# Kernel tuning notes

Hardware: AMD Instinct MI355X
Metric: run time of the kernel (lower is better)

The kernel has to match this reference:

```python
import jax, jax.numpy as jnp
import numpy as np

B, T, D, H = 4, 1024, 1024, 16
DK = D // H
SCALE = float(np.sqrt(DK))


def setup_inputs() -> dict:
    key = jax.random.key(0)
    ks = jax.random.split(key, 12)
    std = 1.0 / np.sqrt(D)
    inp = {
        "x": jax.random.normal(ks[0], (B, T, D), dtype=jnp.float32),
        "s2_distances": jax.random.uniform(ks[1], (B, T, T), dtype=jnp.float32),
        # causal mask: 1 where attention allowed (j <= i)
        "mask": jnp.broadcast_to(jnp.tril(jnp.ones((T, T), dtype=jnp.int32)), (B, T, T)),
        "Wq": jax.random.uniform(ks[2], (D, D), jnp.float32, -std, std),
        "bq": jax.random.uniform(ks[3], (D,), jnp.float32, -std, std),
        "Wk": jax.random.uniform(ks[4], (D, D), jnp.float32, -std, std),
        "bk": jax.random.uniform(ks[5], (D,), jnp.float32, -std, std),
        "Wv": jax.random.uniform(ks[6], (D, D), jnp.float32, -std, std),
        "bv": jax.random.uniform(ks[7], (D,), jnp.float32, -std, std),
        "Wo": jax.random.uniform(ks[8], (D, D), jnp.float32, -std, std),
        "bo": jax.random.uniform(ks[9], (D,), jnp.float32, -std, std),
        "spatial_weight": jnp.float32(0.5),
    }
    return inp


def reference(x, s2_distances, mask, Wq, bq, Wk, bk, Wv, bv, Wo, bo, spatial_weight):
    b, t, _ = x.shape
    # projections: torch nn.Linear is x @ W.T + b
    def proj(W, bias):
        y = jnp.einsum("btd,ed->bte", x, W) + bias
        return y.reshape(b, t, H, DK).transpose(0, 2, 1, 3)  # [B,H,T,dk]

    Q, K, V = proj(Wq, bq), proj(Wk, bk), proj(Wv, bv)
    # scores: QK^T/sqrt(dk) - |alpha| * dist  (dist broadcast over heads)
    scores = jnp.einsum("bhqd,bhkd->bhqk", Q, K) / SCALE
    scores = scores - jnp.abs(spatial_weight) * s2_distances[:, None, :, :]
    scores = jnp.where(mask[:, None, :, :] == 0, -jnp.inf, scores)
    probs = jax.nn.softmax(scores, axis=-1)
    out = jnp.einsum("bhqk,bhkd->bhqd", probs, V)
    out = out.transpose(0, 2, 1, 3).reshape(b, t, D)
    return jnp.einsum("btd,ed->bte", out, Wo) + bo
```

## Files before the change

### kernel.cpp

```cpp
#include <hip/hip_runtime.h>
#include <stdint.h>

#define Tt 1024
#define Dd 1024
#define Hh 16

typedef unsigned short u16;
typedef __attribute__((ext_vector_type(8))) short short8;
typedef __attribute__((ext_vector_type(4))) float f32x4;
typedef __attribute__((ext_vector_type(4))) unsigned short u16x4;

typedef const __attribute__((address_space(1))) uint32_t* gptr_t;
typedef __attribute__((address_space(3))) uint32_t* lptr_t;

#define QSCALE 0.18033688011112042f
#define LOG2E 1.4426950408889634f

static __device__ __forceinline__ u16 f2bf(float f) {
  union { float f; unsigned u; } x;
  x.f = f;
  unsigned u = x.u;
  return (u16)((u + 0x7fffu + ((u >> 16) & 1u)) >> 16);
}

static __device__ __forceinline__ u16 f2bf_fast(float f) {
  union { float f; unsigned u; } x;
  x.f = f;
  return (u16)((x.u + 0x8000u) >> 16);
}

static __device__ __forceinline__ float bf2f(u16 u) {
  union { unsigned u; float f; } x;
  x.u = ((unsigned)u) << 16;
  return x.f;
}

static __device__ __forceinline__ float fexp2(float x) {
#if __has_builtin(__builtin_amdgcn_exp2f)
  return __builtin_amdgcn_exp2f(x);
#else
  return exp2f(x);
#endif
}

__global__ __launch_bounds__(256) void cvt_kernel(
    const float* __restrict__ x, const float* __restrict__ wq,
    const float* __restrict__ wk, const float* __restrict__ wv,
    const float* __restrict__ wo, u16* __restrict__ xb, u16* __restrict__ wb) {
  size_t i = ((size_t)blockIdx.x * 256 + threadIdx.x) * 4;
  const size_t XN = (size_t)4 * 1024 * 1024;
  const float* src;
  u16* dst;
  size_t off;
  if (i < XN) {
    src = x; dst = xb; off = i;
  } else {
    size_t j = i - XN;
    int wi = (int)(j >> 20);
    src = (wi == 0) ? wq : (wi == 1) ? wk : (wi == 2) ? wv : wo;
    dst = wb + ((size_t)wi << 20);
    off = j & ((1u << 20) - 1);
  }
  float4 v = *(const float4*)(src + off);
  u16x4 o;
  o.x = f2bf(v.x); o.y = f2bf(v.y); o.z = f2bf(v.z); o.w = f2bf(v.w);
  *(u16x4*)(dst + off) = o;
}

__global__ __launch_bounds__(512, 2) void qkv_fused_kernel(
    const u16* __restrict__ xb, const u16* __restrict__ wb,
    const float* __restrict__ bq, const float* __restrict__ bk,
    const float* __restrict__ bv, u16* __restrict__ Q, u16* __restrict__ Kk,
    u16* __restrict__ Vt, const float* __restrict__ dist,
    const float* __restrict__ alphap, u16* __restrict__ biasb) {
  __shared__ u16 lds[65536];
  const int bid = blockIdx.x;
  if (bid >= 192) {
    const int cid = bid - 192;
    const float scl = -fabsf(alphap[0]) * LOG2E;
    const size_t id = (size_t)cid * 512 + threadIdx.x;
#pragma unroll 4
    for (int i = 0; i < 32; i++) {
      const size_t off = id * 4 + (size_t)i * 131072;
      float4 v = *(const float4*)(dist + off);
      u16x4 o;
      o.x = f2bf(v.x * scl); o.y = f2bf(v.y * scl);
      o.z = f2bf(v.z * scl); o.w = f2bf(v.w * scl);
      *(u16x4*)(biasb + off) = o;
    }
    return;
  }
  const int mt = bid & 15, ny = bid >> 4;
  const int z = ny >> 2;
  const int m0 = mt * 256, nc = (ny & 3) * 256;
  const u16* W = wb + ((size_t)z << 20);

  const int t = threadIdx.x, w = t >> 6, l = t & 63;
  const int quad = l >> 4, l15 = l & 15;
  const int wr = w >> 2, wn = w & 3;
  char* ldc = (char*)lds;

  const int srow = w * 16 + ((l >> 3) & 7);
  const int schunk = ((l & 7) ^ ((l >> 3) & 7)) * 8;
  const u16* gA = xb + (size_t)(m0 + srow) * Dd + schunk;
  const u16* gB = W + (size_t)(nc + srow) * Dd + schunk;

  auto stage = [&](int kt, int h) {
    const size_t ro = (size_t)(h * 128) * Dd + (size_t)kt * 64;
    char* base = ldc + ((((kt & 1) << 1) | h) * 32768) + w * 2048;
#pragma unroll
    for (int i = 0; i < 2; i++) {
      __builtin_amdgcn_global_load_lds((gptr_t)(gA + ro + (size_t)i * 8 * Dd),
                                       (lptr_t)(base + i * 1024), 16, 0, 0);
      __builtin_amdgcn_global_load_lds((gptr_t)(gB + ro + (size_t)i * 8 * Dd),
                                       (lptr_t)(base + 16384 + i * 1024), 16, 0, 0);
    }
  };

  f32x4 acc[8][4];
#pragma unroll
  for (int i = 0; i < 8; i++)
#pragma unroll
    for (int j = 0; j < 4; j++) acc[i][j] = (f32x4){0.f, 0.f, 0.f, 0.f};

  stage(0, 0); stage(0, 1);
  stage(1, 0); stage(1, 1);
  asm volatile("s_waitcnt vmcnt(8)" ::: "memory");
  __builtin_amdgcn_s_barrier();

  const int swl = l15 & 7;

#pragma unroll 1
  for (int kt = 0; kt < 16; kt++) {
    const char* slA = ldc + ((((kt & 1) << 1) | wr) * 32768);
    const char* slB = ldc + ((((kt & 1) << 1) | (wn >> 1)) * 32768) + 16384;
    const int rB = (wn & 1) * 64;
    {
      short8 af[8], bfv[4];
      const int cs = ((0 * 4 + quad) ^ swl) * 16;
#pragma unroll
      for (int mi = 0; mi < 8; mi++)
        af[mi] = *(const short8*)(slA + (mi * 16 + l15) * 128 + cs);
#pragma unroll
      for (int ni = 0; ni < 4; ni++)
        bfv[ni] = *(const short8*)(slB + (rB + ni * 16 + l15) * 128 + cs);
      __builtin_amdgcn_s_barrier();
      asm volatile("s_waitcnt lgkmcnt(0)" ::: "memory");
      __builtin_amdgcn_sched_barrier(0);
      __builtin_amdgcn_s_setprio(1);
#pragma unroll
      for (int mi = 0; mi < 8; mi++)
#pragma unroll
        for (int ni = 0; ni < 4; ni++)
          acc[mi][ni] = __builtin_amdgcn_mfma_f32_16x16x32_bf16(
              af[mi], bfv[ni], acc[mi][ni], 0, 0, 0);
      __builtin_amdgcn_s_setprio(0);
    }
    {
      short8 af[8], bfv[4];
      const int cs = ((1 * 4 + quad) ^ swl) * 16;
#pragma unroll
      for (int mi = 0; mi < 8; mi++)
        af[mi] = *(const short8*)(slA + (mi * 16 + l15) * 128 + cs);
#pragma unroll
      for (int ni = 0; ni < 4; ni++)
        bfv[ni] = *(const short8*)(slB + (rB + ni * 16 + l15) * 128 + cs);
      __builtin_amdgcn_s_barrier();
      if (kt + 2 < 16) { stage(kt + 2, 0); stage(kt + 2, 1); }
      asm volatile("s_waitcnt lgkmcnt(0)" ::: "memory");
      __builtin_amdgcn_sched_barrier(0);
      __builtin_amdgcn_s_setprio(1);
#pragma unroll
      for (int mi = 0; mi < 8; mi++)
#pragma unroll
        for (int ni = 0; ni < 4; ni++)
          acc[mi][ni] = __builtin_amdgcn_mfma_f32_16x16x32_bf16(
              af[mi], bfv[ni], acc[mi][ni], 0, 0, 0);
      __builtin_amdgcn_s_setprio(0);
      if (kt < 14) {
        asm volatile("s_waitcnt vmcnt(8)" ::: "memory");
      } else if (kt == 14) {
        asm volatile("s_waitcnt vmcnt(0)" ::: "memory");
      }
      if (kt < 15) __builtin_amdgcn_s_barrier();
    }
  }

  const float* bias = (z == 0) ? bq : (z == 1) ? bk : bv;
  const float scl = (z == 0) ? QSCALE : 1.0f;
  if (z < 2) {
#pragma unroll
    for (int mi = 0; mi < 8; mi++)
#pragma unroll
      for (int ni = 0; ni < 4; ni++) {
        const int n = wn * 64 + ni * 16 + l15;
        const float bn = bias[nc + n];
        const int nsw = n ^ (quad << 4);
#pragma unroll
        for (int r = 0; r < 4; r++) {
          const int m = wr * 128 + mi * 16 + quad * 4 + r;
          lds[m * 256 + nsw] = f2bf((acc[mi][ni][r] + bn) * scl);
        }
      }
  } else {
#pragma unroll
    for (int mi = 0; mi < 8; mi++)
#pragma unroll
      for (int ni = 0; ni < 4; ni++) {
        const int n = wn * 64 + ni * 16 + l15;
        const float bn = bias[nc + n];
        u16x4 o;
        o.x = f2bf(acc[mi][ni][0] + bn);
        o.y = f2bf(acc[mi][ni][1] + bn);
        o.z = f2bf(acc[mi][ni][2] + bn);
        o.w = f2bf(acc[mi][ni][3] + bn);
        const int mp = (wr * 128 + mi * 16 + quad * 4) ^ ((n & 7) * 8);
        *(u16x4*)&lds[n * 256 + mp] = o;
      }
  }
  __syncthreads();
  const int row = t >> 5;
  const int c8 = (t & 31) * 8;
  if (z < 2) {
    u16* out = (z == 0) ? Q : Kk;
#pragma unroll
    for (int it = 0; it < 16; it++) {
      const int rr = it * 16 + row;
      const int pos = c8 ^ ((((rr >> 2) & 3)) << 4);
      *(short8*)(out + (size_t)(m0 + rr) * Dd + nc + c8) =
          *(const short8*)&lds[rr * 256 + pos];
    }
  } else {
    const int b2 = m0 >> 10, t0 = m0 & (Tt - 1);
#pragma unroll
    for (int it = 0; it < 16; it++) {
      const int rr = it * 16 + row;
      const int pos = c8 ^ ((rr & 7) * 8);
      *(short8*)(Vt + ((size_t)b2 * Dd + nc + rr) * Tt + t0 + c8) =
          *(const short8*)&lds[rr * 256 + pos];
    }
  }
}

__global__ __launch_bounds__(512) void gemm_out_kernel(
    const u16* __restrict__ Ao, const u16* __restrict__ Wo,
    const float* __restrict__ bo, float* __restrict__ out) {
  __shared__ u16 lds[2 * 12288];
  const int m0 = blockIdx.x * 128, n0 = blockIdx.y * 64;
  const int t = threadIdx.x, w = t >> 6, l = t & 63, quad = l >> 4, l15 = l & 15;
  const int srow = t >> 3;
  const int scol = ((l & 7) ^ ((l >> 3) & 7)) * 8;
  const u16* ga = Ao + (size_t)(m0 + srow) * Dd + scol;
  const u16* gb = Wo + (size_t)(n0 + srow) * Dd + scol;
  char* ldc = (char*)lds;
  const int xr = l15 & 7;
  f32x4 acc[4];
#pragma unroll
  for (int j = 0; j < 4; j++) acc[j] = (f32x4){0.f, 0.f, 0.f, 0.f};

  auto stage = [&](int k0, int buf) {
    char* base = ldc + buf * 24576 + w * 1024;
#pragma unroll
    for (int i = 0; i < 2; i++)
      __builtin_amdgcn_global_load_lds((gptr_t)(ga + k0 + (size_t)i * 64 * Dd),
                                       (lptr_t)(base + i * 8192), 16, 0, 0);
    __builtin_amdgcn_global_load_lds((gptr_t)(gb + k0),
                                     (lptr_t)(base + 16384), 16, 0, 0);
  };

  stage(0, 0);
#pragma unroll 1
  for (int it = 0; it < Dd / 64; it++) {
    const int buf = it & 1;
    __builtin_amdgcn_s_waitcnt(0);
    __syncthreads();
    if (it + 1 < Dd / 64) stage((it + 1) * 64, buf ^ 1);
    const u16* lA = lds + buf * 12288;
    const u16* lB = lA + 8192;
#pragma unroll
    for (int kk = 0; kk < 2; kk++) {
      const int cs = ((kk * 4 + quad) ^ xr) * 8;
      const short8 af = *(const short8*)(lA + (w * 16 + l15) * 64 + cs);
#pragma unroll
      for (int ni = 0; ni < 4; ni++) {
        const short8 bfr = *(const short8*)(lB + (ni * 16 + l15) * 64 + cs);
        acc[ni] = __builtin_amdgcn_mfma_f32_16x16x32_bf16(af, bfr, acc[ni], 0, 0, 0);
      }
    }
  }
#pragma unroll
  for (int ni = 0; ni < 4; ni++) {
    const int n = n0 + ni * 16 + l15;
    const float bn = bo[n];
#pragma unroll
    for (int r = 0; r < 4; r++) {
      const int m = m0 + w * 16 + quad * 4 + r;
      out[(size_t)m * Dd + n] = acc[ni][r] + bn;
    }
  }
}

__global__ __launch_bounds__(256) void attn_kernel(
    const u16* __restrict__ Q, const u16* __restrict__ Kk,
    const u16* __restrict__ Vt, const u16* __restrict__ biasb,
    u16* __restrict__ Oo) {
  __shared__ u16 lK[2][64 * 64];
  __shared__ u16 lV[2][64 * 64];
  __shared__ u16 lPp[4][16 * 64];
  const int t = threadIdx.x, w = t >> 6, l = t & 63, quad = l >> 4, l15 = l & 15;
  const int g = blockIdx.x >> 8;
  const int j = (blockIdx.x >> 6) & 3;
  const int bh = blockIdx.x & 63;
  const int qb = (g == 0) ? 15 - j : (g == 1) ? 8 + j : (g == 2) ? 7 - j : j;
  const int h = bh & (Hh - 1), b = bh >> 4;
  const int q0 = qb * 64;

  const int srow = w * 8 + (l >> 3);
  const int schunk = ((l & 7) ^ ((l >> 3) & 7)) * 8;
  const u16* gK = Kk + ((size_t)b * Tt + srow) * Dd + h * 64 + schunk;
  const u16* gV = Vt + ((size_t)b * Dd + h * 64 + srow) * Tt + schunk;
  char* lKc0 = (char*)&lK[0][0];
  char* lVc0 = (char*)&lV[0][0];
  const int wbase = w * 1024;

  auto stage = [&](int k0, int buf) {
#pragma unroll
    for (int i = 0; i < 2; i++) {
      __builtin_amdgcn_global_load_lds(
          (gptr_t)(gK + (size_t)(k0 + i * 32) * Dd),
          (lptr_t)(lKc0 + buf * 8192 + wbase + i * 4096), 16, 0, 0);
      __builtin_amdgcn_global_load_lds(
          (gptr_t)(gV + (size_t)(i * 32) * Tt + k0),
          (lptr_t)(lVc0 + buf * 8192 + wbase + i * 4096), 16, 0, 0);
    }
  };

  const int qrow = q0 + w * 16 + l15;
  const u16* Qp = Q + ((size_t)b * Tt + qrow) * Dd + h * 64 + quad * 8;
  const short8 qf0 = *(const short8*)Qp;
  const short8 qf1 = *(const short8*)(Qp + 32);
  const u16* bp = biasb + ((size_t)b * Tt + qrow) * Tt + quad * 4;

  const int xr = l15 & 7;
  u16* lpr = &lPp[w][l15 * 64];
  const int niter = qb + 1;

  f32x4 oacc[4];
#pragma unroll
  for (int dt = 0; dt < 4; dt++) oacc[dt] = (f32x4){0.f, 0.f, 0.f, 0.f};
  f32x4 lsum4 = (f32x4){0.f, 0.f, 0.f, 0.f};
  u16x4 bbA[4], bbB[4];

  stage(0, 0);
#pragma unroll
  for (int nt = 0; nt < 4; nt++) bbA[nt] = *(const u16x4*)(bp + nt * 16);

#pragma unroll 1
  for (int kt = 0; kt < niter; kt++) {
    const int buf = kt & 1;
    __builtin_amdgcn_s_waitcnt(0);
    __syncthreads();
    if (kt + 1 < niter) {
      stage((kt + 1) * 64, buf ^ 1);
#pragma unroll
      for (int nt = 0; nt < 4; nt++)
        bbB[nt] = *(const u16x4*)(bp + (kt + 1) * 64 + nt * 16);
    }
    f32x4 sacc[4];
#pragma unroll
    for (int nt = 0; nt < 4; nt++) {
#pragma unroll
      for (int r = 0; r < 4; r++) sacc[nt][r] = bf2f(bbA[nt][r]);
    }
#pragma unroll
    for (int ks = 0; ks < 2; ks++) {
      const short8 qf = ks ? qf1 : qf0;
      const int cs = ((ks * 4 + quad) ^ xr) * 8;
#pragma unroll
      for (int nt = 0; nt < 4; nt++) {
        const short8 kf = *(const short8*)&lK[buf][(nt * 16 + l15) * 64 + cs];
        sacc[nt] = __builtin_amdgcn_mfma_f32_16x16x32_bf16(kf, qf, sacc[nt], 0, 0, 0);
      }
    }
    if (kt == qb) {
      const int kbase = kt * 64 + quad * 4;
#pragma unroll
      for (int nt = 0; nt < 4; nt++) {
        u16x4 pk;
#pragma unroll
        for (int r = 0; r < 4; r++) {
          const float p = (kbase + nt * 16 + r <= qrow) ? fexp2(sacc[nt][r]) : 0.f;
          lsum4[nt] += p;
          pk[r] = f2bf_fast(p);
        }
        *(u16x4*)&lpr[((nt * 4 + quad) ^ (xr << 1)) * 4] = pk;
      }
    } else {
#pragma unroll
      for (int nt = 0; nt < 4; nt++) {
        u16x4 pk;
#pragma unroll
        for (int r = 0; r < 4; r++) {
          const float p = fexp2(sacc[nt][r]);
          lsum4[nt] += p;
          pk[r] = f2bf_fast(p);
        }
        *(u16x4*)&lpr[((nt * 4 + quad) ^ (xr << 1)) * 4] = pk;
      }
    }
#pragma unroll
    for (int ks = 0; ks < 2; ks++) {
      const int cs = ((ks * 4 + quad) ^ xr) * 8;
      const short8 pa = *(const short8*)&lpr[cs];
#pragma unroll
      for (int dt = 0; dt < 4; dt++) {
        const short8 vf = *(const short8*)&lV[buf][(dt * 16 + l15) * 64 + cs];
        oacc[dt] = __builtin_amdgcn_mfma_f32_16x16x32_bf16(pa, vf, oacc[dt], 0, 0, 0);
      }
    }
#pragma unroll
    for (int nt = 0; nt < 4; nt++) bbA[nt] = bbB[nt];
  }

  float lsum = (lsum4[0] + lsum4[1]) + (lsum4[2] + lsum4[3]);
  lsum += __shfl_xor(lsum, 16);
  lsum += __shfl_xor(lsum, 32);
  const float inv = 1.0f / lsum;
  float invq[4];
#pragma unroll
  for (int r = 0; r < 4; r++) invq[r] = __shfl(inv, quad * 4 + r);
#pragma unroll
  for (int dt = 0; dt < 4; dt++) {
#pragma unroll
    for (int r = 0; r < 4; r++) {
      Oo[((size_t)b * Tt + q0 + w * 16 + quad * 4 + r) * Dd + h * 64 + dt * 16 + l15] =
          f2bf(oacc[dt][r] * invq[r]);
    }
  }
}

extern "C" void kernel_launch(void* const* d_in, const int* in_sizes, int n_in,
                              void* d_out, int out_size, void* d_ws, size_t ws_size,
                              hipStream_t stream) {
  const float* x = (const float*)d_in[0];
  const float* dist = (const float*)d_in[1];
  const float* Wq = (const float*)d_in[3];
  const float* bq = (const float*)d_in[4];
  const float* Wk = (const float*)d_in[5];
  const float* bk = (const float*)d_in[6];
  const float* Wv = (const float*)d_in[7];
  const float* bv = (const float*)d_in[8];
  const float* Wo = (const float*)d_in[9];
  const float* bo = (const float*)d_in[10];
  const float* alphap = (const float*)d_in[11];

  char* ws = (char*)d_ws;
  u16* xb = (u16*)(ws);
  u16* wb = (u16*)(ws + ((size_t)8 << 20));
  u16* Qb = (u16*)(ws + ((size_t)16 << 20));
  u16* Kb = (u16*)(ws + ((size_t)24 << 20));
  u16* Vtb = (u16*)(ws + ((size_t)32 << 20));
  u16* biasb = (u16*)(ws + ((size_t)40 << 20));
  u16* Ob = xb;
  float* outp = (float*)d_out;

  cvt_kernel<<<8192, 256, 0, stream>>>(x, Wq, Wk, Wv, Wo, xb, wb);
  qkv_fused_kernel<<<256, 512, 0, stream>>>(xb, wb, bq, bk, bv, Qb, Kb, Vtb,
                                            dist, alphap, biasb);
  attn_kernel<<<1024, 256, 0, stream>>>(Qb, Kb, Vtb, biasb, Ob);
  dim3 g2(32, 16);
  gemm_out_kernel<<<g2, 512, 0, stream>>>(Ob, wb + ((size_t)3 << 20), bo, outp);
}
```

Before: 191.3 us.

## Enlarge output GEMM tile to 128x128 with register-prefetched LDS pipeline

Rewrites the output projection GEMM to use 128x128 tiles on 256 blocks instead of 128x64 tiles on 512 blocks. Each wave now computes a 64x32 sub-tile, which gives more MFMA reuse per LDS fragment load. Fragments are loaded into registers before the barrier so the next-next stage's global-to-LDS copy can be issued early, using vmcnt-based waits and a priority boost around the MFMAs. The cost is fewer blocks (256 across the CUs) and higher register pressure, and the hand-written waitcnt logic is fragile.

Result: no change. 192.7 us (+0.8%).

```diff
diff --git a/kernel.cpp b/kernel.cpp
--- a/kernel.cpp
+++ b/kernel.cpp
@@ -245,59 +245,92 @@
 __global__ __launch_bounds__(512) void gemm_out_kernel(
     const u16* __restrict__ Ao, const u16* __restrict__ Wo,
     const float* __restrict__ bo, float* __restrict__ out) {
-  __shared__ u16 lds[2 * 12288];
-  const int m0 = blockIdx.x * 128, n0 = blockIdx.y * 64;
-  const int t = threadIdx.x, w = t >> 6, l = t & 63, quad = l >> 4, l15 = l & 15;
-  const int srow = t >> 3;
-  const int scol = ((l & 7) ^ ((l >> 3) & 7)) * 8;
-  const u16* ga = Ao + (size_t)(m0 + srow) * Dd + scol;
-  const u16* gb = Wo + (size_t)(n0 + srow) * Dd + scol;
+  __shared__ u16 lds[32768];
+  const int mt = blockIdx.x & 31, ny = blockIdx.x >> 5;
+  const int m0 = mt * 128, n0 = ny * 128;
+  const int t = threadIdx.x, w = t >> 6, l = t & 63;
+  const int quad = l >> 4, l15 = l & 15;
+  const int wr = w >> 2, wn = w & 3;
   char* ldc = (char*)lds;
-  const int xr = l15 & 7;
-  f32x4 acc[4];
-#pragma unroll
-  for (int j = 0; j < 4; j++) acc[j] = (f32x4){0.f, 0.f, 0.f, 0.f};
-
-  auto stage = [&](int k0, int buf) {
-    char* base = ldc + buf * 24576 + w * 1024;
-#pragma unroll
-    for (int i = 0; i < 2; i++)
-      __builtin_amdgcn_global_load_lds((gptr_t)(ga + k0 + (size_t)i * 64 * Dd),
-                                       (lptr_t)(base + i * 8192), 16, 0, 0);
-    __builtin_amdgcn_global_load_lds((gptr_t)(gb + k0),
-                                     (lptr_t)(base + 16384), 16, 0, 0);
+
+  const int srow = w * 8 + (l >> 3);
+  const int schunk = ((l & 7) ^ ((l >> 3) & 7)) * 8;
+  const u16* gA = Ao + (size_t)(m0 + srow) * Dd + schunk;
+  const u16* gB = Wo + (size_t)(n0 + srow) * Dd + schunk;
+
+  auto stage = [&](int kt) {
+    char* base = ldc + (kt & 1) * 32768 + w * 1024;
+#pragma unroll
+    for (int i = 0; i < 2; i++) {
+      __builtin_amdgcn_global_load_lds(
+          (gptr_t)(gA + (size_t)i * 64 * Dd + (size_t)kt * 64),
+          (lptr_t)(base + i * 8192), 16, 0, 0);
+      __builtin_amdgcn_global_load_lds(
+          (gptr_t)(gB + (size_t)i * 64 * Dd + (size_t)kt * 64),
+          (lptr_t)(base + 16384 + i * 8192), 16, 0, 0);
+    }
   };
 
-  stage(0, 0);
+  f32x4 acc[4][2];
+#pragma unroll
+  for (int i = 0; i < 4; i++)
+#pragma unroll
+    for (int j = 0; j < 2; j++) acc[i][j] = (f32x4){0.f, 0.f, 0.f, 0.f};
+
+  stage(0); stage(1);
+  asm volatile("s_waitcnt vmcnt(4)" ::: "memory");
+  __builtin_amdgcn_s_barrier();
+
+  const int swl = l15 & 7;
+
 #pragma unroll 1
-  for (int it = 0; it < Dd / 64; it++) {
-    const int buf = it & 1;
-    __builtin_amdgcn_s_waitcnt(0);
-    __syncthreads();
-    if (it + 1 < Dd / 64) stage((it + 1) * 64, buf ^ 1);
-    const u16* lA = lds + buf * 12288;
-    const u16* lB = lA + 8192;
-#pragma unroll
-    for (int kk = 0; kk < 2; kk++) {
-      const int cs = ((kk * 4 + quad) ^ xr) * 8;
-      const short8 af = *(const short8*)(lA + (w * 16 + l15) * 64 + cs);
-#pragma unroll
-      for (int ni = 0; ni < 4; ni++) {
-        const short8 bfr = *(const short8*)(lB + (ni * 16 + l15) * 64 + cs);
-        acc[ni] = __builtin_amdgcn_mfma_f32_16x16x32_bf16(af, bfr, acc[ni], 0, 0, 0);
-      }
-    }
-  }
-#pragma unroll
-  for (int ni = 0; ni < 4; ni++) {
-    const int n = n0 + ni * 16 + l15;
-    const float bn = bo[n];
-#pragma unroll
-    for (int r = 0; r < 4; r++) {
-      const int m = m0 + w * 16 + quad * 4 + r;
-      out[(size_t)m * Dd + n] = acc[ni][r] + bn;
-    }
-  }
+  for (int kt = 0; kt < 16; kt++) {
+    const char* sl = ldc + (kt & 1) * 32768;
+    short8 af[2][4], bfv[2][2];
+#pragma unroll
+    for (int ks = 0; ks < 2; ks++) {
+      const int cs = ((ks * 4 + quad) ^ swl) * 16;
+#pragma unroll
+      for (int mi = 0; mi < 4; mi++)
+        af[ks][mi] = *(const short8*)(sl + (wr * 64 + mi * 16 + l15) * 128 + cs);
+#pragma unroll
+      for (int ni = 0; ni < 2; ni++)
+        bfv[ks][ni] = *(const short8*)(sl + 16384 + (wn * 32 + ni * 16 + l15) * 128 + cs);
+    }
+    __builtin_amdgcn_s_barrier();
+    if (kt + 2 < 16) stage(kt + 2);
+    asm volatile("s_waitcnt lgkmcnt(0)" ::: "memory");
+    __builtin_amdgcn_sched_barrier(0);
+    __builtin_amdgcn_s_setprio(1);
+#pragma unroll
+    for (int ks = 0; ks < 2; ks++)
+#pragma unroll
+      for (int mi = 0; mi < 4; mi++)
+#pragma unroll
+        for (int ni = 0; ni < 2; ni++)
+          acc[mi][ni] = __builtin_amdgcn_mfma_f32_16x16x32_bf16(
+              af[ks][mi], bfv[ks][ni], acc[mi][ni], 0, 0, 0);
+    __builtin_amdgcn_s_setprio(0);
+    if (kt < 14) {
+      asm volatile("s_waitcnt vmcnt(4)" ::: "memory");
+    } else if (kt == 14) {
+      asm volatile("s_waitcnt vmcnt(0)" ::: "memory");
+    }
+    if (kt < 15) __builtin_amdgcn_s_barrier();
+  }
+
+#pragma unroll
+  for (int mi = 0; mi < 4; mi++)
+#pragma unroll
+    for (int ni = 0; ni < 2; ni++) {
+      const int n = n0 + wn * 32 + ni * 16 + l15;
+      const float bn = bo[n];
+#pragma unroll
+      for (int r = 0; r < 4; r++) {
+        const int m = m0 + wr * 64 + mi * 16 + quad * 4 + r;
+        out[(size_t)m * Dd + n] = acc[mi][ni][r] + bn;
+      }
+    }
 }
 
 __global__ __launch_bounds__(256) void attn_kernel(
@@ -468,6 +501,5 @@
   qkv_fused_kernel<<<256, 512, 0, stream>>>(xb, wb, bq, bk, bv, Qb, Kb, Vtb,
                                             dist, alphap, biasb);
   attn_kernel<<<1024, 256, 0, stream>>>(Qb, Kb, Vtb, biasb, Ob);
-  dim3 g2(32, 16);
-  gemm_out_kernel<<<g2, 512, 0, stream>>>(Ob, wb + ((size_t)3 << 20), bo, outp);
-}
+  gemm_out_kernel<<<256, 512, 0, stream>>>(Ob, wb + ((size_t)3 << 20), bo, outp);
+}
```
